# Performance work log

Hardware: AMD Instinct MI355X
Metric: run time of the kernel (lower is better)

Reference implementation:

```python
import jax, jax.numpy as jnp
import numpy as np

B, N, D, H, IN, HID = 16, 1024, 256, 8, 256, 1024
HD = IN // H  # head dim = 32
EPS = 1e-5


def layer_norm(x, g, b):
    mu = jnp.mean(x, axis=-1, keepdims=True)
    var = jnp.var(x, axis=-1, keepdims=True)
    return (x - mu) / jnp.sqrt(var + EPS) * g + b


def setup_inputs() -> dict:
    key = jax.random.key(0)
    ks = jax.random.split(key, 12)
    s = 0.02
    return {
        "x": jax.random.normal(ks[0], (B, N, D), jnp.float32),
        "coords": jax.random.normal(ks[1], (B, N, 2), jnp.float32),
        "g1": jnp.ones((D,), jnp.float32),
        "b1": jnp.zeros((D,), jnp.float32),
        "Wqkv": jax.random.normal(ks[2], (3 * IN, D), jnp.float32) * s,
        "Wproj": jax.random.normal(ks[3], (IN, IN), jnp.float32) * s,
        "bproj": jnp.zeros((IN,), jnp.float32),
        "g2": jnp.ones((D,), jnp.float32),
        "b2": jnp.zeros((D,), jnp.float32),
        "W1": jax.random.normal(ks[4], (HID, D), jnp.float32) * s,
        "bb1": jnp.zeros((HID,), jnp.float32),
        "W2": jax.random.normal(ks[5], (D, HID), jnp.float32) * s,
        "bb2": jnp.zeros((D,), jnp.float32),
    }


def reference(x, coords, g1, b1, Wqkv, Wproj, bproj, g2, b2, W1, bb1, W2, bb2):
    # ---- Attention branch (pre-norm) ----
    h = layer_norm(x, g1, b1)                       # [B,N,D]
    qkv = h @ Wqkv.T                                # [B,N,3*IN]
    qkv = qkv.reshape(B, N, 3, H, HD).transpose(2, 0, 3, 1, 4)  # [3,B,H,N,HD]
    q, k, v = qkv[0], qkv[1], qkv[2]
    scale = HD ** -0.5
    attn = jnp.einsum('bhid,bhjd->bhij', q * scale, k)  # [B,H,N,N]
    attn = jax.nn.softmax(attn, axis=-1)
    o = jnp.einsum('bhij,bhjd->bhid', attn, v)      # [B,H,N,HD]
    o = o.transpose(0, 2, 1, 3).reshape(B, N, IN)   # [B,N,IN]
    o = o @ Wproj.T + bproj
    o = o + h                                       # residual inside Attention (vs normed input)
    x = x + o                                       # Block residual (double residual, faithful)
    # ---- MLP branch ----
    h2 = layer_norm(x, g2, b2)
    m = jax.nn.gelu(h2 @ W1.T + bb1, approximate=False) @ W2.T + bb2
    return x + m
```

## Files before the change

### kernel.cpp

```cpp
#include <hip/hip_runtime.h>
#include <hip/hip_bf16.h>
#include <math.h>

#define Bdim 16
#define Ndim 1024
#define Ddim 256
#define Hdim 8
#define HDdim 32
#define INdim 256
#define HIDdim 1024
#define Tdim (Bdim * Ndim)

typedef __attribute__((ext_vector_type(8)))  short bf16x8;
typedef __attribute__((ext_vector_type(4)))  short bf16x4;
typedef __attribute__((ext_vector_type(16))) float f32x16;
typedef unsigned int u32;

__device__ inline short f2bf(float x) {
    union { __hip_bfloat16 b; short s; } u;
    u.b = __float2bfloat16(x);
    return u.s;
}

__device__ inline float bf2f(short s) {
    return __uint_as_float(((u32)(unsigned short)s) << 16);
}

__device__ inline float fexp2(float x) {
#if __has_builtin(__builtin_amdgcn_exp2f)
    return __builtin_amdgcn_exp2f(x);
#else
    return exp2f(x);
#endif
}

__device__ inline u32 pack2bf(float a, float b) {
#if __has_builtin(__builtin_amdgcn_cvt_pk_bf16_f32)
    typedef __attribute__((ext_vector_type(2))) __bf16 bf16x2_t;
    union { bf16x2_t v; u32 u; } c;
    c.v = __builtin_amdgcn_cvt_pk_bf16_f32(a, b);
    return c.u;
#else
    u32 ua = __float_as_uint(a), ub = __float_as_uint(b);
    return ((ua + 0x8000u) >> 16) | ((ub + 0x8000u) & 0xffff0000u);
#endif
}

__device__ inline void plswap(u32 &a, u32 &b) {
    asm volatile("v_permlane32_swap_b32 %0, %1" : "+v"(a), "+v"(b));
}

__device__ inline float gelu_exact(float v) {
    return 0.5f * v * (1.0f + erff(v * 0.70710678118654752f));
}

#define N4_QKV  (3 * INdim * Ddim / 4)
#define N4_PROJ (INdim * INdim / 4)
#define N4_W1   (HIDdim * Ddim / 4)
#define N4_W2   (Ddim * HIDdim / 4)

__global__ __launch_bounds__(256) void cvt_all_kernel(const float* __restrict__ s0,
                                                      const float* __restrict__ s1,
                                                      const float* __restrict__ s2,
                                                      const float* __restrict__ s3,
                                                      short* __restrict__ d0,
                                                      short* __restrict__ d1,
                                                      short* __restrict__ d2,
                                                      short* __restrict__ d3) {
    int i = blockIdx.x * 256 + threadIdx.x;
    const float* src; short* dst; int j;
    if (i < N4_QKV)                          { src = s0; dst = d0; j = i; }
    else if (i < N4_QKV + N4_PROJ)           { src = s1; dst = d1; j = i - N4_QKV; }
    else if (i < N4_QKV + N4_PROJ + N4_W1)   { src = s2; dst = d2; j = i - N4_QKV - N4_PROJ; }
    else                                     { src = s3; dst = d3; j = i - N4_QKV - N4_PROJ - N4_W1; }
    float4 v = ((const float4*)src)[j];
    bf16x4 b;
    b[0] = f2bf(v.x); b[1] = f2bf(v.y); b[2] = f2bf(v.z); b[3] = f2bf(v.w);
    ((bf16x4*)dst)[j] = b;
}

__global__ __launch_bounds__(256) void ln4_kernel(const float* __restrict__ x,
                                                  const float* __restrict__ g,
                                                  const float* __restrict__ b,
                                                  float* __restrict__ outf,
                                                  short* __restrict__ outb) {
    int w = threadIdx.x >> 6, lane = threadIdx.x & 63;
    int row = blockIdx.x * 4 + w;
    float4 v = ((const float4*)x)[(size_t)row * 64 + lane];
    float s  = (v.x + v.y) + (v.z + v.w);
    float s2 = (v.x * v.x + v.y * v.y) + (v.z * v.z + v.w * v.w);
    #pragma unroll
    for (int off = 32; off; off >>= 1) {
        s  += __shfl_xor(s,  off, 64);
        s2 += __shfl_xor(s2, off, 64);
    }
    float mu   = s * (1.0f / Ddim);
    float var  = s2 * (1.0f / Ddim) - mu * mu;
    float rstd = rsqrtf(var + 1e-5f);
    float4 gg = ((const float4*)g)[lane];
    float4 bb = ((const float4*)b)[lane];
    float4 r;
    r.x = (v.x - mu) * rstd * gg.x + bb.x;
    r.y = (v.y - mu) * rstd * gg.y + bb.y;
    r.z = (v.z - mu) * rstd * gg.z + bb.z;
    r.w = (v.w - mu) * rstd * gg.w + bb.w;
    if (outf) ((float4*)outf)[(size_t)row * 64 + lane] = r;
    bf16x4 rb;
    rb[0] = f2bf(r.x); rb[1] = f2bf(r.y); rb[2] = f2bf(r.z); rb[3] = f2bf(r.w);
    ((bf16x4*)outb)[(size_t)row * 64 + lane] = rb;
}

#define EPI_NONE 0
#define EPI_PROJ 1
#define EPI_GELU 2
#define EPI_RES  3
#define EPI_QKV  4

#define GPAD32 40
#define SCALE2Q 0.25505654249892417f

__device__ inline bf16x8 comb8(bf16x8 a, bf16x8 b, float rl) {
    bf16x8 r;
    #pragma unroll
    for (int i = 0; i < 8; ++i) r[i] = f2bf((bf2f(a[i]) + bf2f(b[i])) * rl);
    return r;
}

template <int EPI, int BN, bool COMB>
__global__ __launch_bounds__(256) void gemm_mfma(const short* __restrict__ A,
                                                 const short* __restrict__ W,
                                                 void* __restrict__ Cv,
                                                 int M, int N, int K,
                                                 const float* __restrict__ bias,
                                                 const float* __restrict__ add1,
                                                 const float* __restrict__ add2,
                                                 const float* __restrict__ lpc) {
    __shared__ short As[64 * GPAD32];
    __shared__ short Bs[BN * GPAD32];
    const int tid = threadIdx.x, w = tid >> 6, lane = tid & 63;
    const int col = lane & 31;
    const int half_id = lane >> 5;

    const int nbx = gridDim.x;
    const int flat = blockIdx.y * nbx + blockIdx.x;
    const int cpx = (nbx * (int)gridDim.y) >> 3;
    const int swz = (flat & 7) * cpx + (flat >> 3);
    const int m0 = (swz / nbx) * 64, n0 = (swz % nbx) * BN;

    const int wm = (w & 1) * 32;
    const int wn = (BN == 128) ? (w >> 1) * 64 : (w >> 1) * 32;
    constexpr int TN = (BN == 128) ? 2 : 1;

    f32x16 acc[TN];
    #pragma unroll
    for (int t = 0; t < TN; ++t) acc[t] = 0.0f;

    const int sra = tid >> 2, ssa = (tid & 3) * 8;
    const int srb = (BN == 128) ? (tid >> 1) : (tid >> 2);
    const int ssb = (BN == 128) ? (tid & 1) * 16 : (tid & 3) * 8;
    constexpr int NB = (BN == 128) ? 2 : 1;

    const short* pAsrc = &A[(size_t)(m0 + sra) * K + ssa];
    const short* pBsrc = &W[(size_t)(n0 + srb) * K + ssb];
    const float* lpr0 = COMB ? (lpc + (size_t)(m0 + sra) * 8) : nullptr;
    const float* lpr1 = COMB ? (lpr0 + (size_t)Tdim * 8) : nullptr;

    bf16x8 pa, pa2, pb[NB];
    float pl = 0.0f;
    pa = *(const bf16x8*)&pAsrc[0];
    if constexpr (COMB) {
        pa2 = *(const bf16x8*)(pAsrc + (size_t)Tdim * 256);
        pl = lpr0[0] + lpr1[0];
    }
    #pragma unroll
    for (int j = 0; j < NB; ++j) pb[j] = *(const bf16x8*)&pBsrc[j * 8];

    const int T = K >> 5;
    for (int kt = 0; kt < T; ++kt) {
        __syncthreads();
        {
            bf16x8 av = pa;
            if constexpr (COMB) av = comb8(pa, pa2, 1.0f / pl);
            *(bf16x8*)&As[sra * GPAD32 + ssa] = av;
        }
        #pragma unroll
        for (int j = 0; j < NB; ++j) *(bf16x8*)&Bs[srb * GPAD32 + ssb + j * 8] = pb[j];
        __syncthreads();

        if (kt + 1 < T) {
            const short* a = pAsrc + (kt + 1) * 32;
            const short* b = pBsrc + (kt + 1) * 32;
            pa = *(const bf16x8*)&a[0];
            if constexpr (COMB) {
                pa2 = *(const bf16x8*)(a + (size_t)Tdim * 256);
                pl = lpr0[kt + 1] + lpr1[kt + 1];
            }
            #pragma unroll
            for (int j = 0; j < NB; ++j) pb[j] = *(const bf16x8*)&b[j * 8];
        }

        #pragma unroll
        for (int ks = 0; ks < 2; ++ks) {
            bf16x8 af = *(const bf16x8*)&As[(wm + col) * GPAD32 + ks * 16 + half_id * 8];
            bf16x8 bfv[TN];
            #pragma unroll
            for (int t = 0; t < TN; ++t)
                bfv[t] = *(const bf16x8*)&Bs[(wn + t * 32 + col) * GPAD32 + ks * 16 + half_id * 8];
            #pragma unroll
            for (int t = 0; t < TN; ++t)
                acc[t] = __builtin_amdgcn_mfma_f32_32x32x16_bf16(af, bfv[t], acc[t], 0, 0, 0);
        }
    }

    float* Cf = (float*)Cv;
    short* Cb = (short*)Cv;
    #pragma unroll
    for (int r = 0; r < 16; ++r) {
        int row = m0 + wm + (r & 3) + 8 * (r >> 2) + 4 * half_id;
        #pragma unroll
        for (int t = 0; t < TN; ++t) {
            int cn = n0 + wn + t * 32 + col;
            size_t off = (size_t)row * N + cn;
            float v = acc[t][r];
            if (EPI != EPI_NONE && EPI != EPI_QKV) v += bias[cn];
            if (EPI == EPI_QKV && cn < 256) v *= SCALE2Q;
            if (EPI == EPI_GELU) v = gelu_exact(v);
            if (EPI == EPI_PROJ) v += add1[off] + add2[off];
            if (EPI == EPI_RES)  v += add1[off];
            if (EPI == EPI_PROJ || EPI == EPI_RES) Cf[off] = v;
            else                                   Cb[off] = f2bf(v);
        }
    }
}

#define VTPAD 136

__global__ __launch_bounds__(256) void vtrans_kernel(const short* __restrict__ qkv,
                                                     short* __restrict__ vT) {
    __shared__ short Tl[32 * VTPAD];
    const int tid = threadIdx.x;
    const int bh = blockIdx.x, c = blockIdx.y;
    const int b = bh >> 3, head = bh & 7;
    {
        int r = tid >> 1, hv = tid & 1;
        const short* src = qkv + (size_t)b * Ndim * 768 + (size_t)(c * 128 + r) * 768
                           + 512 + head * 32 + hv * 16;
        bf16x8 v0 = *(const bf16x8*)&src[0];
        bf16x8 v1 = *(const bf16x8*)&src[8];
        #pragma unroll
        for (int i = 0; i < 8; ++i) {
            Tl[(hv * 16 + i) * VTPAD + r]     = v0[i];
            Tl[(hv * 16 + 8 + i) * VTPAD + r] = v1[i];
        }
    }
    __syncthreads();
    {
        int d = tid >> 3, j16 = (tid & 7) * 16;
        short* dst = vT + (size_t)(bh * 32 + d) * Ndim + c * 128 + j16;
        *(bf16x8*)&dst[0] = *(const bf16x8*)&Tl[d * VTPAD + j16];
        *(bf16x8*)&dst[8] = *(const bf16x8*)&Tl[d * VTPAD + j16 + 8];
    }
}

#define KVPAD 40
#define CHUNK 128

__global__ __launch_bounds__(256) void attn_mfma_kernel(const short* __restrict__ qkv,
                                                        const short* __restrict__ vT,
                                                        short* __restrict__ opart,
                                                        float* __restrict__ lpart) {
    __shared__ short Ks[CHUNK * KVPAD];
    __shared__ short Vt[32 * VTPAD];

    const int tid = threadIdx.x;
    const int w = tid >> 6;
    const int lane = tid & 63;
    const int col = lane & 31;
    const int half_id = lane >> 5;

    const int id = blockIdx.x;
    const int xcd = id & 7;
    const int s_ = id >> 3;
    const int bh = ((s_ >> 4) << 3) | xcd;
    const int qp = s_ & 15;
    const int qblk = qp & 7;
    const int part = qp >> 3;

    const int b = bh >> 3, head = bh & 7;
    const int q0w = qblk * 128 + w * 32;

    const size_t qkvb = (size_t)b * Ndim * 768;
    short* op = opart + (size_t)part * Tdim * 256;
    float* lp = lpart + (size_t)part * Tdim * 8;

    const int sr = tid >> 1, shv = tid & 1;
    const short* ksrc = qkv + qkvb + (size_t)sr * 768 + 256 + head * 32 + shv * 16;
    const int sd = tid >> 3, sj16 = (tid & 7) * 16;
    const short* vsrc = vT + (size_t)(bh * 32 + sd) * Ndim + sj16;

    bf16x8 qf[2];
    {
        const short* qrow = qkv + qkvb + (size_t)(q0w + col) * 768 + head * 32;
        #pragma unroll
        for (int kh = 0; kh < 2; ++kh)
            qf[kh] = *(const bf16x8*)&qrow[kh * 16 + half_id * 8];
    }

    bf16x8 vone;
    #pragma unroll
    for (int i = 0; i < 8; ++i) vone[i] = (short)0x3F80;

    f32x16 o_acc = 0.0f, l_acc = 0.0f;

    const int c0 = part * 4;

    bf16x8 rk0, rk1, rv0, rv1;
    {
        const short* kp = ksrc + (size_t)(c0 * CHUNK) * 768;
        rk0 = *(const bf16x8*)&kp[0];
        rk1 = *(const bf16x8*)&kp[8];
        const short* vp = vsrc + c0 * CHUNK;
        rv0 = *(const bf16x8*)&vp[0];
        rv1 = *(const bf16x8*)&vp[8];
    }

    #pragma unroll
    for (int ci = 0; ci < 4; ++ci) {
        if (ci != 0) __syncthreads();
        *(bf16x8*)&Ks[sr * KVPAD + shv * 16]     = rk0;
        *(bf16x8*)&Ks[sr * KVPAD + shv * 16 + 8] = rk1;
        *(bf16x8*)&Vt[sd * VTPAD + sj16]     = rv0;
        *(bf16x8*)&Vt[sd * VTPAD + sj16 + 8] = rv1;
        __syncthreads();

        if (ci < 3) {
            const short* kp = ksrc + (size_t)((c0 + ci + 1) * CHUNK) * 768;
            rk0 = *(const bf16x8*)&kp[0];
            rk1 = *(const bf16x8*)&kp[8];
            const short* vp = vsrc + (c0 + ci + 1) * CHUNK;
            rv0 = *(const bf16x8*)&vp[0];
            rv1 = *(const bf16x8*)&vp[8];
        }

        f32x16 s_cur;
        {
            bf16x8 kf0 = *(bf16x8*)&Ks[col * KVPAD + half_id * 8];
            bf16x8 kf1 = *(bf16x8*)&Ks[col * KVPAD + 16 + half_id * 8];
            f32x16 z = 0.0f;
            z = __builtin_amdgcn_mfma_f32_32x32x16_bf16(kf0, qf[0], z, 0, 0, 0);
            z = __builtin_amdgcn_mfma_f32_32x32x16_bf16(kf1, qf[1], z, 0, 0, 0);
            s_cur = z;
        }
        #pragma unroll
        for (int jt = 0; jt < 4; ++jt) {
            f32x16 s_next;
            if (jt < 3) {
                bf16x8 kf0 = *(bf16x8*)&Ks[((jt + 1) * 32 + col) * KVPAD + half_id * 8];
                bf16x8 kf1 = *(bf16x8*)&Ks[((jt + 1) * 32 + col) * KVPAD + 16 + half_id * 8];
                f32x16 z = 0.0f;
                z = __builtin_amdgcn_mfma_f32_32x32x16_bf16(kf0, qf[0], z, 0, 0, 0);
                z = __builtin_amdgcn_mfma_f32_32x32x16_bf16(kf1, qf[1], z, 0, 0, 0);
                s_next = z;
            }

            bf16x8 vf0 = *(bf16x8*)&Vt[col * VTPAD + jt * 32 + half_id * 8];
            bf16x8 vf1 = *(bf16x8*)&Vt[col * VTPAD + jt * 32 + 16 + half_id * 8];

            u32 wd[8];
            #pragma unroll
            for (int g = 0; g < 8; ++g) {
                float e0 = fexp2(s_cur[2 * g + 0]);
                float e1 = fexp2(s_cur[2 * g + 1]);
                wd[g] = pack2bf(e0, e1);
            }
            plswap(wd[0], wd[2]); plswap(wd[1], wd[3]);
            plswap(wd[4], wd[6]); plswap(wd[5], wd[7]);

            union { u32 u[4]; bf16x8 v; } p0, p1;
            p0.u[0] = wd[0]; p0.u[1] = wd[1]; p0.u[2] = wd[2]; p0.u[3] = wd[3];
            p1.u[0] = wd[4]; p1.u[1] = wd[5]; p1.u[2] = wd[6]; p1.u[3] = wd[7];

            __builtin_amdgcn_s_setprio(1);
            o_acc = __builtin_amdgcn_mfma_f32_32x32x16_bf16(p0.v, vf0, o_acc, 0, 0, 0);
            o_acc = __builtin_amdgcn_mfma_f32_32x32x16_bf16(p1.v, vf1, o_acc, 0, 0, 0);
            l_acc = __builtin_amdgcn_mfma_f32_32x32x16_bf16(p0.v, vone, l_acc, 0, 0, 0);
            l_acc = __builtin_amdgcn_mfma_f32_32x32x16_bf16(p1.v, vone, l_acc, 0, 0, 0);
            __builtin_amdgcn_s_setprio(0);

            if (jt < 3) s_cur = s_next;
        }
    }

    #pragma unroll
    for (int r = 0; r < 16; ++r) {
        int q_r = (r & 3) + 8 * (r >> 2) + 4 * half_id;
        size_t gq = (size_t)(b * Ndim + q0w + q_r);
        op[gq * INdim + head * 32 + col] = f2bf(o_acc[r]);
    }
    if (col < 16) {
        int r = col;
        int q_r = (r & 3) + 8 * (r >> 2) + 4 * half_id;
        lp[(size_t)(b * Ndim + q0w + q_r) * 8 + head] = l_acc[r];
    }
}

extern "C" void kernel_launch(void* const* d_in, const int* in_sizes, int n_in,
                              void* d_out, int out_size, void* d_ws, size_t ws_size,
                              hipStream_t stream) {
    const float* x     = (const float*)d_in[0];
    const float* g1    = (const float*)d_in[2];
    const float* b1    = (const float*)d_in[3];
    const float* Wqkv  = (const float*)d_in[4];
    const float* Wproj = (const float*)d_in[5];
    const float* bproj = (const float*)d_in[6];
    const float* g2    = (const float*)d_in[7];
    const float* b2    = (const float*)d_in[8];
    const float* W1    = (const float*)d_in[9];
    const float* bb1   = (const float*)d_in[10];
    const float* W2    = (const float*)d_in[11];
    const float* bb2   = (const float*)d_in[12];
    float* out = (float*)d_out;

    char* ws = (char*)d_ws;
    float* h      = (float*)(ws);
    short* h_bf   = (short*)(ws + (size_t)(16u << 20));
    short* qkv_bf = (short*)(ws + (size_t)(24u << 20));
    float* xnew   = (float*)(ws + (size_t)(24u << 20));
    short* opart  = (short*)(ws + (size_t)(48u << 20));
    short* mid_bf = (short*)(ws + (size_t)(48u << 20));
    float* lpart  = (float*)(ws + (size_t)(80u << 20));
    short* vT     = (short*)(ws + (size_t)(81u << 20));
    short* wqkv_b = (short*)(ws + (size_t)(89u << 20));
    short* wproj_b= (short*)(ws + (size_t)(89u << 20) + 768 * 1024);
    short* w1_b   = (short*)(ws + (size_t)(90u << 20));
    short* w2_b   = (short*)(ws + (size_t)(90u << 20) + 512 * 1024);

    cvt_all_kernel<<<(N4_QKV + N4_PROJ + N4_W1 + N4_W2 + 255) / 256, 256, 0, stream>>>(
        Wqkv, Wproj, W1, W2, wqkv_b, wproj_b, w1_b, w2_b);

    ln4_kernel<<<Tdim / 4, 256, 0, stream>>>(x, g1, b1, h, h_bf);
    gemm_mfma<EPI_QKV, 128, false><<<dim3(768 / 128, Tdim / 64), 256, 0, stream>>>(
        h_bf, wqkv_b, qkv_bf, Tdim, 768, 256, nullptr, nullptr, nullptr, nullptr);
    vtrans_kernel<<<dim3(Bdim * Hdim, Ndim / 128), 256, 0, stream>>>(qkv_bf, vT);
    attn_mfma_kernel<<<2048, 256, 0, stream>>>(qkv_bf, vT, opart, lpart);
    gemm_mfma<EPI_PROJ, 64, true><<<dim3(256 / 64, Tdim / 64), 256, 0, stream>>>(
        opart, wproj_b, xnew, Tdim, 256, 256, bproj, h, x, lpart);
    ln4_kernel<<<Tdim / 4, 256, 0, stream>>>(xnew, g2, b2, nullptr, h_bf);
    gemm_mfma<EPI_GELU, 128, false><<<dim3(1024 / 128, Tdim / 64), 256, 0, stream>>>(
        h_bf, w1_b, mid_bf, Tdim, 1024, 256, bb1, nullptr, nullptr, nullptr);
    gemm_mfma<EPI_RES, 64, false><<<dim3(256 / 64, Tdim / 64), 256, 0, stream>>>(
        mid_bf, w2_b, out, Tdim, 256, 1024, bb2, xnew, nullptr, nullptr);
}
```

Before: 214.7 us.

## Use direct global-to-LDS loads with double-buffered, swizzled tiles in GEMMs

Adds a GEMM path that stages A and W tiles through global_load_lds straight into LDS. The tiles are double-buffered, so the next K-slice loads while MFMAs consume the current one, with one barrier per iteration instead of two. LDS rows are unpadded and use an XOR swizzle on 16-byte chunks to avoid bank conflicts, and the register round-trip for staging is gone. It is enabled for the QKV, MLP1 and MLP2 GEMMs but not the projection, which needs the combine step. It doubles LDS use per block and relies on the wave-uniform LDS destination semantics of the builtin.

```diff
diff --git a/kernel.cpp b/kernel.cpp
--- a/kernel.cpp
+++ b/kernel.cpp
@@ -52,6 +52,12 @@
 
 __device__ inline float gelu_exact(float v) {
     return 0.5f * v * (1.0f + erff(v * 0.70710678118654752f));
+}
+
+typedef __attribute__((address_space(1))) const u32 gas_t;
+typedef __attribute__((address_space(3))) u32 las_t;
+__device__ inline void gl16(const short* g, short* l) {
+    __builtin_amdgcn_global_load_lds((gas_t*)g, (las_t*)l, 16, 0, 0);
 }
 
 #define N4_QKV  (3 * INdim * Ddim / 4)
@@ -126,7 +132,7 @@
     return r;
 }
 
-template <int EPI, int BN, bool COMB>
+template <int EPI, int BN, bool COMB, bool GL>
 __global__ __launch_bounds__(256) void gemm_mfma(const short* __restrict__ A,
                                                  const short* __restrict__ W,
                                                  void* __restrict__ Cv,
@@ -135,8 +141,10 @@
                                                  const float* __restrict__ add1,
                                                  const float* __restrict__ add2,
                                                  const float* __restrict__ lpc) {
-    __shared__ short As[64 * GPAD32];
-    __shared__ short Bs[BN * GPAD32];
+    constexpr int AP = GL ? 32 : GPAD32;
+    constexpr int NB2 = GL ? 2 : 1;
+    __shared__ short As[NB2][64 * AP];
+    __shared__ short Bs[NB2][BN * AP];
     const int tid = threadIdx.x, w = tid >> 6, lane = tid & 63;
     const int col = lane & 31;
     const int half_id = lane >> 5;
@@ -155,60 +163,112 @@
     #pragma unroll
     for (int t = 0; t < TN; ++t) acc[t] = 0.0f;
 
-    const int sra = tid >> 2, ssa = (tid & 3) * 8;
-    const int srb = (BN == 128) ? (tid >> 1) : (tid >> 2);
-    const int ssb = (BN == 128) ? (tid & 1) * 16 : (tid & 3) * 8;
-    constexpr int NB = (BN == 128) ? 2 : 1;
-
-    const short* pAsrc = &A[(size_t)(m0 + sra) * K + ssa];
-    const short* pBsrc = &W[(size_t)(n0 + srb) * K + ssb];
-    const float* lpr0 = COMB ? (lpc + (size_t)(m0 + sra) * 8) : nullptr;
-    const float* lpr1 = COMB ? (lpr0 + (size_t)Tdim * 8) : nullptr;
-
-    bf16x8 pa, pa2, pb[NB];
-    float pl = 0.0f;
-    pa = *(const bf16x8*)&pAsrc[0];
-    if constexpr (COMB) {
-        pa2 = *(const bf16x8*)(pAsrc + (size_t)Tdim * 256);
-        pl = lpr0[0] + lpr1[0];
-    }
-    #pragma unroll
-    for (int j = 0; j < NB; ++j) pb[j] = *(const bf16x8*)&pBsrc[j * 8];
-
     const int T = K >> 5;
-    for (int kt = 0; kt < T; ++kt) {
-        __syncthreads();
-        {
-            bf16x8 av = pa;
-            if constexpr (COMB) av = comb8(pa, pa2, 1.0f / pl);
-            *(bf16x8*)&As[sra * GPAD32 + ssa] = av;
+
+    if constexpr (GL) {
+        const int srow = lane >> 2;
+        const int schk = (lane & 3) ^ ((lane >> 3) & 3);
+        const short* gA = &A[(size_t)(m0 + w * 16 + srow) * K + schk * 8];
+        const short* gB0;
+        const short* gB1 = nullptr;
+        if constexpr (BN == 128) {
+            gB0 = &W[(size_t)(n0 + w * 32 + srow) * K + schk * 8];
+            gB1 = &W[(size_t)(n0 + w * 32 + 16 + srow) * K + schk * 8];
+        } else {
+            gB0 = &W[(size_t)(n0 + w * 16 + srow) * K + schk * 8];
+        }
+
+        auto STAGE = [&](int buf, int kt) {
+            gl16(gA + kt * 32, &As[buf][w * 512]);
+            if constexpr (BN == 128) {
+                gl16(gB0 + kt * 32, &Bs[buf][w * 1024]);
+                gl16(gB1 + kt * 32, &Bs[buf][w * 1024 + 512]);
+            } else {
+                gl16(gB0 + kt * 32, &Bs[buf][w * 512]);
+            }
+        };
+
+        STAGE(0, 0);
+        asm volatile("s_waitcnt vmcnt(0)" ::: "memory");
+        __builtin_amdgcn_s_barrier();
+
+        int cur = 0;
+        for (int kt = 0; kt < T; ++kt) {
+            if (kt + 1 < T) STAGE(cur ^ 1, kt + 1);
+            #pragma unroll
+            for (int ks = 0; ks < 2; ++ks) {
+                const int c = ks * 2 + half_id;
+                const int Ra = wm + col;
+                bf16x8 af = *(const bf16x8*)&As[cur][Ra * 32 + (c ^ ((Ra >> 1) & 3)) * 8];
+                bf16x8 bfv[TN];
+                #pragma unroll
+                for (int t = 0; t < TN; ++t) {
+                    const int Rb = wn + t * 32 + col;
+                    bfv[t] = *(const bf16x8*)&Bs[cur][Rb * 32 + (c ^ ((Rb >> 1) & 3)) * 8];
+                }
+                #pragma unroll
+                for (int t = 0; t < TN; ++t)
+                    acc[t] = __builtin_amdgcn_mfma_f32_32x32x16_bf16(af, bfv[t], acc[t], 0, 0, 0);
+            }
+            asm volatile("s_waitcnt vmcnt(0)" ::: "memory");
+            __builtin_amdgcn_s_barrier();
+            cur ^= 1;
+        }
+    } else {
+        const int sra = tid >> 2, ssa = (tid & 3) * 8;
+        const int srb = (BN == 128) ? (tid >> 1) : (tid >> 2);
+        const int ssb = (BN == 128) ? (tid & 1) * 16 : (tid & 3) * 8;
+        constexpr int NB = (BN == 128) ? 2 : 1;
+
+        const short* pAsrc = &A[(size_t)(m0 + sra) * K + ssa];
+        const short* pBsrc = &W[(size_t)(n0 + srb) * K + ssb];
+        const float* lpr0 = COMB ? (lpc + (size_t)(m0 + sra) * 8) : nullptr;
+        const float* lpr1 = COMB ? (lpr0 + (size_t)Tdim * 8) : nullptr;
+
+        bf16x8 pa, pa2, pb[NB];
+        float pl = 0.0f;
+        pa = *(const bf16x8*)&pAsrc[0];
+        if constexpr (COMB) {
+            pa2 = *(const bf16x8*)(pAsrc + (size_t)Tdim * 256);
+            pl = lpr0[0] + lpr1[0];
         }
         #pragma unroll
-        for (int j = 0; j < NB; ++j) *(bf16x8*)&Bs[srb * GPAD32 + ssb + j * 8] = pb[j];
-        __syncthreads();
-
-        if (kt + 1 < T) {
-            const short* a = pAsrc + (kt + 1) * 32;
-            const short* b = pBsrc + (kt + 1) * 32;
-            pa = *(const bf16x8*)&a[0];
-            if constexpr (COMB) {
-                pa2 = *(const bf16x8*)(a + (size_t)Tdim * 256);
-                pl = lpr0[kt + 1] + lpr1[kt + 1];
+        for (int j = 0; j < NB; ++j) pb[j] = *(const bf16x8*)&pBsrc[j * 8];
+
+        for (int kt = 0; kt < T; ++kt) {
+            __syncthreads();
+            {
+                bf16x8 av = pa;
+                if constexpr (COMB) av = comb8(pa, pa2, 1.0f / pl);
+                *(bf16x8*)&As[0][sra * GPAD32 + ssa] = av;
             }
             #pragma unroll
-            for (int j = 0; j < NB; ++j) pb[j] = *(const bf16x8*)&b[j * 8];
-        }
-
-        #pragma unroll
-        for (int ks = 0; ks < 2; ++ks) {
-            bf16x8 af = *(const bf16x8*)&As[(wm + col) * GPAD32 + ks * 16 + half_id * 8];
-            bf16x8 bfv[TN];
+            for (int j = 0; j < NB; ++j) *(bf16x8*)&Bs[0][srb * GPAD32 + ssb + j * 8] = pb[j];
+            __syncthreads();
+
+            if (kt + 1 < T) {
+                const short* a = pAsrc + (kt + 1) * 32;
+                const short* b = pBsrc + (kt + 1) * 32;
+                pa = *(const bf16x8*)&a[0];
+                if constexpr (COMB) {
+                    pa2 = *(const bf16x8*)(a + (size_t)Tdim * 256);
+                    pl = lpr0[kt + 1] + lpr1[kt + 1];
+                }
+                #pragma unroll
+                for (int j = 0; j < NB; ++j) pb[j] = *(const bf16x8*)&b[j * 8];
+            }
+
             #pragma unroll
-            for (int t = 0; t < TN; ++t)
-                bfv[t] = *(const bf16x8*)&Bs[(wn + t * 32 + col) * GPAD32 + ks * 16 + half_id * 8];
-            #pragma unroll
-            for (int t = 0; t < TN; ++t)
-                acc[t] = __builtin_amdgcn_mfma_f32_32x32x16_bf16(af, bfv[t], acc[t], 0, 0, 0);
+            for (int ks = 0; ks < 2; ++ks) {
+                bf16x8 af = *(const bf16x8*)&As[0][(wm + col) * GPAD32 + ks * 16 + half_id * 8];
+                bf16x8 bfv[TN];
+                #pragma unroll
+                for (int t = 0; t < TN; ++t)
+                    bfv[t] = *(const bf16x8*)&Bs[0][(wn + t * 32 + col) * GPAD32 + ks * 16 + half_id * 8];
+                #pragma unroll
+                for (int t = 0; t < TN; ++t)
+                    acc[t] = __builtin_amdgcn_mfma_f32_32x32x16_bf16(af, bfv[t], acc[t], 0, 0, 0);
+            }
         }
     }
 
@@ -439,15 +499,15 @@
         Wqkv, Wproj, W1, W2, wqkv_b, wproj_b, w1_b, w2_b);
 
     ln4_kernel<<<Tdim / 4, 256, 0, stream>>>(x, g1, b1, h, h_bf);
-    gemm_mfma<EPI_QKV, 128, false><<<dim3(768 / 128, Tdim / 64), 256, 0, stream>>>(
+    gemm_mfma<EPI_QKV, 128, false, true><<<dim3(768 / 128, Tdim / 64), 256, 0, stream>>>(
         h_bf, wqkv_b, qkv_bf, Tdim, 768, 256, nullptr, nullptr, nullptr, nullptr);
     vtrans_kernel<<<dim3(Bdim * Hdim, Ndim / 128), 256, 0, stream>>>(qkv_bf, vT);
     attn_mfma_kernel<<<2048, 256, 0, stream>>>(qkv_bf, vT, opart, lpart);
-    gemm_mfma<EPI_PROJ, 64, true><<<dim3(256 / 64, Tdim / 64), 256, 0, stream>>>(
+    gemm_mfma<EPI_PROJ, 64, true, false><<<dim3(256 / 64, Tdim / 64), 256, 0, stream>>>(
         opart, wproj_b, xnew, Tdim, 256, 256, bproj, h, x, lpart);
     ln4_kernel<<<Tdim / 4, 256, 0, stream>>>(xnew, g2, b2, nullptr, h_bf);
-    gemm_mfma<EPI_GELU, 128, false><<<dim3(1024 / 128, Tdim / 64), 256, 0, stream>>>(
+    gemm_mfma<EPI_GELU, 128, false, true><<<dim3(1024 / 128, Tdim / 64), 256, 0, stream>>>(
         h_bf, w1_b, mid_bf, Tdim, 1024, 256, bb1, nullptr, nullptr, nullptr);
-    gemm_mfma<EPI_RES, 64, false><<<dim3(256 / 64, Tdim / 64), 256, 0, stream>>>(
+    gemm_mfma<EPI_RES, 64, false, true><<<dim3(256 / 64, Tdim / 64), 256, 0, stream>>>(
         mid_bf, w2_b, out, Tdim, 256, 1024, bb2, xnew, nullptr, nullptr);
 }
```

Result: no change. 216.9 us (+1.0%).

## Add 128x128 tiled GEMM with direct global-to-LDS loads for QKV and MLP1

Applied to the files above, without the earlier changes.

Adds a new bf16 MFMA GEMM kernel using 128x128 output tiles, a K-step of 64, XOR-swizzled LDS layout, and global_load_lds direct copies. Block indices are also remapped in a grouped swizzle to improve L2 reuse. It replaces the 64-row-tile GEMM for the QKV and first MLP projections, aiming to raise arithmetic intensity and cut load instruction overhead. The loop is single-buffered with two barriers per K step, so load latency is not overlapped with compute. The Q scaling moves into the new kernel, which leaves that branch unused in the old one.

```diff
diff --git a/kernel.cpp b/kernel.cpp
--- a/kernel.cpp
+++ b/kernel.cpp
@@ -52,6 +52,12 @@
 
 __device__ inline float gelu_exact(float v) {
     return 0.5f * v * (1.0f + erff(v * 0.70710678118654752f));
+}
+
+typedef __attribute__((address_space(1))) const u32 gas_t;
+typedef __attribute__((address_space(3))) u32 las_t;
+__device__ inline void gl16(const short* g, short* l) {
+    __builtin_amdgcn_global_load_lds((gas_t*)g, (las_t*)l, 16, 0, 0);
 }
 
 #define N4_QKV  (3 * INdim * Ddim / 4)
@@ -116,8 +122,88 @@
 #define EPI_RES  3
 #define EPI_QKV  4
 
+#define SCALE2Q 0.25505654249892417f
+
+template <int EPI>
+__global__ __launch_bounds__(256) void gemm128(const short* __restrict__ A,
+                                               const short* __restrict__ W,
+                                               short* __restrict__ C,
+                                               int N, int K,
+                                               const float* __restrict__ bias) {
+    __shared__ __attribute__((aligned(16))) short As[128 * 64];
+    __shared__ __attribute__((aligned(16))) short Bs[128 * 64];
+    const int tid = threadIdx.x, w = tid >> 6, lane = tid & 63;
+    const int col = lane & 31;
+    const int half_id = lane >> 5;
+
+    const int nbx = gridDim.x;
+    const int flat = blockIdx.y * nbx + blockIdx.x;
+    const int cpx = (nbx * (int)gridDim.y) >> 3;
+    const int swz = (flat & 7) * cpx + (flat >> 3);
+    const int m0 = (swz / nbx) * 128, n0 = (swz % nbx) * 128;
+
+    const int wm = (w & 1) * 64;
+    const int wn = (w >> 1) * 64;
+
+    f32x16 acc[2][2];
+    #pragma unroll
+    for (int i = 0; i < 2; ++i) { acc[i][0] = 0.0f; acc[i][1] = 0.0f; }
+
+    const int lrow = lane >> 3;
+    const int lchk = (lane & 7) ^ lrow;
+    const short* gA = &A[(size_t)(m0 + w * 32 + lrow) * K + lchk * 8];
+    const short* gB = &W[(size_t)(n0 + w * 32 + lrow) * K + lchk * 8];
+    short* lA = &As[(w * 32) * 64];
+    short* lB = &Bs[(w * 32) * 64];
+
+    const int T = K >> 6;
+    for (int kt = 0; kt < T; ++kt) {
+        if (kt) __syncthreads();
+        #pragma unroll
+        for (int i = 0; i < 4; ++i) {
+            gl16(gA + (size_t)(i * 8) * K + kt * 64, lA + i * 512);
+            gl16(gB + (size_t)(i * 8) * K + kt * 64, lB + i * 512);
+        }
+        __syncthreads();
+
+        #pragma unroll
+        for (int ks = 0; ks < 4; ++ks) {
+            const int c = ks * 2 + half_id;
+            bf16x8 af[2], bfv[2];
+            #pragma unroll
+            for (int t = 0; t < 2; ++t) {
+                const int Ra = wm + t * 32 + col;
+                af[t] = *(const bf16x8*)&As[Ra * 64 + ((c ^ (Ra & 7)) * 8)];
+                const int Rb = wn + t * 32 + col;
+                bfv[t] = *(const bf16x8*)&Bs[Rb * 64 + ((c ^ (Rb & 7)) * 8)];
+            }
+            #pragma unroll
+            for (int tm = 0; tm < 2; ++tm)
+                #pragma unroll
+                for (int tn = 0; tn < 2; ++tn)
+                    acc[tm][tn] = __builtin_amdgcn_mfma_f32_32x32x16_bf16(
+                        af[tm], bfv[tn], acc[tm][tn], 0, 0, 0);
+        }
+    }
+
+    #pragma unroll
+    for (int tm = 0; tm < 2; ++tm) {
+        #pragma unroll
+        for (int r = 0; r < 16; ++r) {
+            int row = m0 + wm + tm * 32 + (r & 3) + 8 * (r >> 2) + 4 * half_id;
+            #pragma unroll
+            for (int tn = 0; tn < 2; ++tn) {
+                int cn = n0 + wn + tn * 32 + col;
+                float v = acc[tm][tn][r];
+                if (EPI == EPI_QKV && cn < 256) v *= SCALE2Q;
+                if (EPI == EPI_GELU) v = gelu_exact(v + bias[cn]);
+                C[(size_t)row * N + cn] = f2bf(v);
+            }
+        }
+    }
+}
+
 #define GPAD32 40
-#define SCALE2Q 0.25505654249892417f
 
 __device__ inline bf16x8 comb8(bf16x8 a, bf16x8 b, float rl) {
     bf16x8 r;
@@ -223,7 +309,6 @@
             size_t off = (size_t)row * N + cn;
             float v = acc[t][r];
             if (EPI != EPI_NONE && EPI != EPI_QKV) v += bias[cn];
-            if (EPI == EPI_QKV && cn < 256) v *= SCALE2Q;
             if (EPI == EPI_GELU) v = gelu_exact(v);
             if (EPI == EPI_PROJ) v += add1[off] + add2[off];
             if (EPI == EPI_RES)  v += add1[off];
@@ -439,15 +524,15 @@
         Wqkv, Wproj, W1, W2, wqkv_b, wproj_b, w1_b, w2_b);
 
     ln4_kernel<<<Tdim / 4, 256, 0, stream>>>(x, g1, b1, h, h_bf);
-    gemm_mfma<EPI_QKV, 128, false><<<dim3(768 / 128, Tdim / 64), 256, 0, stream>>>(
-        h_bf, wqkv_b, qkv_bf, Tdim, 768, 256, nullptr, nullptr, nullptr, nullptr);
+    gemm128<EPI_QKV><<<dim3(768 / 128, Tdim / 128), 256, 0, stream>>>(
+        h_bf, wqkv_b, qkv_bf, 768, 256, nullptr);
     vtrans_kernel<<<dim3(Bdim * Hdim, Ndim / 128), 256, 0, stream>>>(qkv_bf, vT);
     attn_mfma_kernel<<<2048, 256, 0, stream>>>(qkv_bf, vT, opart, lpart);
     gemm_mfma<EPI_PROJ, 64, true><<<dim3(256 / 64, Tdim / 64), 256, 0, stream>>>(
         opart, wproj_b, xnew, Tdim, 256, 256, bproj, h, x, lpart);
     ln4_kernel<<<Tdim / 4, 256, 0, stream>>>(xnew, g2, b2, nullptr, h_bf);
-    gemm_mfma<EPI_GELU, 128, false><<<dim3(1024 / 128, Tdim / 64), 256, 0, stream>>>(
-        h_bf, w1_b, mid_bf, Tdim, 1024, 256, bb1, nullptr, nullptr, nullptr);
+    gemm128<EPI_GELU><<<dim3(1024 / 128, Tdim / 128), 256, 0, stream>>>(
+        h_bf, w1_b, mid_bf, 1024, 256, bb1);
     gemm_mfma<EPI_RES, 64, false><<<dim3(256 / 64, Tdim / 64), 256, 0, stream>>>(
         mid_bf, w2_b, out, Tdim, 256, 1024, bb2, xnew, nullptr, nullptr);
 }
```

New measurement: 211.2 us. About the same (-1.6%).
